# Kernel tuning notes

Measured on AMD Instinct MI355X. Metric: run time of the kernel, lower is better.

## Reference

```python
import jax, jax.numpy as jnp
import numpy as np

B, N, E = 1, 100000, 1250000
IN, OUT = 128, 64


def setup_inputs() -> dict:
    key = jax.random.key(0)
    k = jax.random.split(key, 5)
    x = jax.random.normal(k[0], (B, N, IN), jnp.float32)
    edge_index = jax.random.randint(k[1], (B, 2, E), 0, N, dtype=jnp.int32)
    rank_mapping = jnp.zeros((2, E), jnp.int32)  # single-rank: all zeros
    W1 = jax.random.normal(k[2], (IN, OUT), jnp.float32) / np.sqrt(IN)
    Wp = jax.random.normal(k[3], (2 * OUT, 1), jnp.float32) / np.sqrt(2 * OUT)
    bp = jnp.zeros((1,), jnp.float32)
    bias = jnp.zeros((OUT,), jnp.float32)
    return {"x": x, "edge_index": edge_index, "rank_mapping": rank_mapping,
            "W1": W1, "Wp": Wp, "bp": bp, "bias": bias}


def reference(x, edge_index, rank_mapping, W1, Wp, bp, bias):
    # x: [B, N, IN]; edge_index: [B, 2, E]
    del rank_mapping  # comm routing metadata; identity on a single rank
    n = x.shape[1]
    h = jnp.einsum('bnf,fo->bno', x, W1)          # conv1 (no bias)
    src = edge_index[:, 0, :]                     # [B, E]
    dst = edge_index[:, 1, :]
    h_i = jnp.take_along_axis(h, dst[..., None], axis=1)   # gather at dst
    h_j = jnp.take_along_axis(h, src[..., None], axis=1)   # gather at src
    messages = jnp.concatenate([h_i, h_j], axis=-1)        # [B, E, 2*OUT]
    s = jnp.einsum('bec,co->beo', messages, Wp) + bp       # project_message
    s = jnp.where(s >= 0, s, 0.2 * s)                      # LeakyReLU(0.2)
    numerator = jnp.exp(s)                                 # [B, E, 1]
    seg = jax.vmap(lambda v, i: jax.ops.segment_sum(v, i, num_segments=n))
    denominator = seg(numerator, dst)                      # [B, N, 1]
    # NOTE: original gathers denominator with the *src* indices — replicated.
    denom_e = jnp.take_along_axis(denominator, src[..., None], axis=1)
    alpha = numerator / (denom_e + 1e-16)                  # [B, E, 1]
    out = seg(h_j * alpha, dst)                            # scatter-aggregate
    return out + bias
```

## Files before the change

### kernel.cpp

```cpp
#include <hip/hip_runtime.h>


#define MAXB 1024
#define EPB 4096
#define BIN_CAP 2560

typedef __attribute__((ext_vector_type(8))) short short8v;
typedef __attribute__((ext_vector_type(4))) float floatx4;

static __device__ __forceinline__ float bf2f(unsigned short u) {
    unsigned v = (unsigned)u << 16;
    return __builtin_bit_cast(float, v);
}
static __device__ __forceinline__ unsigned short f2bf(float f) {
    unsigned u = __builtin_bit_cast(unsigned, f);
    u = (u + 0x7FFFu + ((u >> 16) & 1u)) >> 16;
    return (unsigned short)u;
}

__global__ __launch_bounds__(256) void fused_nt_count_kernel(
    const float* __restrict__ x, const float* __restrict__ W1,
    const float* __restrict__ Wp, const int* __restrict__ ei,
    float* __restrict__ h, float* __restrict__ aArr, float* __restrict__ bArr,
    int* __restrict__ C, int N, int E, int G, int B)
{
    __shared__ __align__(16) unsigned short w1b[4][4][4][16][8];
    __shared__ int cnt[MAXB];
    const int tid = threadIdx.x;

    if (blockIdx.x < G) {
        const int g = blockIdx.x;
        for (int i = tid; i < B; i += 256) cnt[i] = 0;
        __syncthreads();
        const int base = g * EPB;
        #pragma unroll
        for (int k = 0; k < EPB / 256; ++k) {
            int e = base + k * 256 + tid;
            if (e < E) atomicAdd(&cnt[ei[E + e] >> 7], 1);
        }
        __syncthreads();
        for (int i = tid; i < B; i += 256) C[(size_t)g * B + i] = cnt[i];
        return;
    }

    for (int i = tid; i < 128 * 64; i += 256) {
        int k = i >> 6, o = i & 63;
        w1b[k >> 5][o >> 4][(k >> 3) & 3][o & 15][k & 7] = f2bf(W1[i]);
    }

    const int w = tid >> 6, lane = tid & 63;
    const int hi = lane >> 4, col = lane & 15;
    float wpa4[4], wpb4[4];
    #pragma unroll
    for (int ot = 0; ot < 4; ++ot) {
        wpa4[ot] = Wp[ot * 16 + col];
        wpb4[ot] = Wp[64 + ot * 16 + col];
    }
    __syncthreads();

    const int n0 = (blockIdx.x - G) * 64 + w * 16;
    int arow = n0 + col; if (arow >= N) arow = N - 1;
    const float* xrow = x + (size_t)arow * 128 + hi * 8;

    floatx4 acc[4] = {{0.f,0.f,0.f,0.f},{0.f,0.f,0.f,0.f},
                      {0.f,0.f,0.f,0.f},{0.f,0.f,0.f,0.f}};
    #pragma unroll
    for (int kb = 0; kb < 4; ++kb) {
        float4 x0 = *reinterpret_cast<const float4*>(xrow + kb * 32);
        float4 x1 = *reinterpret_cast<const float4*>(xrow + kb * 32 + 4);
        short8v af;
        af[0] = (short)f2bf(x0.x); af[1] = (short)f2bf(x0.y);
        af[2] = (short)f2bf(x0.z); af[3] = (short)f2bf(x0.w);
        af[4] = (short)f2bf(x1.x); af[5] = (short)f2bf(x1.y);
        af[6] = (short)f2bf(x1.z); af[7] = (short)f2bf(x1.w);
        #pragma unroll
        for (int ot = 0; ot < 4; ++ot) {
            short8v bf = *reinterpret_cast<const short8v*>(&w1b[kb][ot][hi][col][0]);
            acc[ot] = __builtin_amdgcn_mfma_f32_16x16x32_bf16(af, bf, acc[ot], 0, 0, 0);
        }
    }

    #pragma unroll
    for (int ot = 0; ot < 4; ++ot) {
        #pragma unroll
        for (int r = 0; r < 4; ++r) {
            int n = n0 + hi * 4 + r;
            if (n < N) h[(size_t)n * 64 + ot * 16 + col] = acc[ot][r];
        }
    }
    #pragma unroll
    for (int r = 0; r < 4; ++r) {
        float pa = acc[0][r] * wpa4[0] + acc[1][r] * wpa4[1]
                 + acc[2][r] * wpa4[2] + acc[3][r] * wpa4[3];
        float pb = acc[0][r] * wpb4[0] + acc[1][r] * wpb4[1]
                 + acc[2][r] * wpb4[2] + acc[3][r] * wpb4[3];
        #pragma unroll
        for (int m = 1; m <= 8; m <<= 1) {
            pa += __shfl_xor(pa, m);
            pb += __shfl_xor(pb, m);
        }
        int n = n0 + hi * 4 + r;
        if (col == r && n < N) { aArr[n] = pa; bArr[n] = pb; }
    }
}

__global__ __launch_bounds__(256) void colscan_kernel(
    int* __restrict__ C, int* __restrict__ S, int G, int B)
{
    __shared__ int s[256];
    const int b = blockIdx.x, t = threadIdx.x;
    int g0 = 2 * t, g1 = 2 * t + 1;
    int c0 = (g0 < G) ? C[(size_t)g0 * B + b] : 0;
    int c1 = (g1 < G) ? C[(size_t)g1 * B + b] : 0;
    int v = c0 + c1;
    s[t] = v;
    __syncthreads();
    for (int off = 1; off < 256; off <<= 1) {
        int u = (t >= off) ? s[t - off] : 0;
        __syncthreads();
        s[t] += u;
        __syncthreads();
    }
    int ex = s[t] - v;
    if (g0 < G) C[(size_t)g0 * B + b] = ex;
    if (g1 < G) C[(size_t)g1 * B + b] = ex + c0;
    if (t == 255) S[b] = s[255];
}

__global__ __launch_bounds__(256) void binscan_kernel(
    const int* __restrict__ S, int* __restrict__ binStart,
    int* __restrict__ offsets, int B, int N, int E)
{
    __shared__ int ts[256];
    const int t = threadIdx.x;
    const int chunk = (B + 255) >> 8;
    const int base = t * chunk, lim = min(B, base + chunk);
    int s = 0;
    for (int i = base; i < lim; ++i) s += S[i];
    ts[t] = s;
    __syncthreads();
    for (int off = 1; off < 256; off <<= 1) {
        int u = (t >= off) ? ts[t - off] : 0;
        __syncthreads();
        ts[t] += u;
        __syncthreads();
    }
    int run = ts[t] - s;
    for (int i = base; i < lim; ++i) { binStart[i] = run; run += S[i]; }
    if (t == 0) { binStart[B] = E; offsets[N] = E; }
}

__global__ __launch_bounds__(256) void pass2_kernel(
    const int* __restrict__ ei, const float* __restrict__ aArr,
    const float* __restrict__ bArr, const float* __restrict__ bp,
    const int* __restrict__ C, const int* __restrict__ binStart,
    int2* __restrict__ staging, int E, int G, int B)
{
    __shared__ int cur[MAXB];
    const int g = blockIdx.x, t = threadIdx.x;
    for (int i = t; i < B; i += 256)
        cur[i] = binStart[i] + C[(size_t)g * B + i];
    __syncthreads();
    const float bp0 = bp[0];
    const int base = g * EPB;
    #pragma unroll
    for (int k = 0; k < EPB / 256; ++k) {
        int e = base + k * 256 + t;
        if (e >= E) break;
        int src = ei[e];
        int dst = ei[E + e];
        float s = aArr[dst] + bArr[src] + bp0;
        s = (s >= 0.f) ? s : 0.2f * s;
        float num = __expf(s);
        int bin = dst >> 7;
        int pos = atomicAdd(&cur[bin], 1);
        staging[pos] = make_int2(((dst & 127) << 17) | src, __float_as_int(num));
    }
}

__global__ __launch_bounds__(256) void localsort_kernel(
    const int* __restrict__ binStart, int2* __restrict__ staging,
    int* __restrict__ offsets, int N)
{
    __shared__ int2 sEnt[BIN_CAP];
    __shared__ int sCnt[256], sScan[256], sCur[128];
    const int b = blockIdx.x, t = threadIdx.x;
    const int sBeg = binStart[b];
    const int count = min(binStart[b + 1] - sBeg, BIN_CAP);

    sCnt[t] = 0;
    if (t < 128) sCur[t] = 0;
    __syncthreads();
    for (int i = t; i < count; i += 256) {
        int2 e = staging[sBeg + i];
        sEnt[i] = e;
        atomicAdd(&sCnt[e.x >> 17], 1);
    }
    __syncthreads();
    int v = sCnt[t];
    sScan[t] = v;
    __syncthreads();
    for (int off = 1; off < 256; off <<= 1) {
        int u = (t >= off) ? sScan[t - off] : 0;
        __syncthreads();
        sScan[t] += u;
        __syncthreads();
    }
    int ex = sScan[t] - v;
    __syncthreads();
    sScan[t] = ex;
    const int n0 = b << 7;
    const int Cl = min(128, N - n0);
    if (t < Cl) offsets[n0 + t] = sBeg + ex;
    __syncthreads();
    for (int i = t; i < count; i += 256) {
        int2 e = sEnt[i];
        int dl = e.x >> 17;
        int pos = sBeg + sScan[dl] + atomicAdd(&sCur[dl], 1);
        staging[pos] = make_int2(e.x & 0x1FFFF, e.y);
    }
}

__global__ __launch_bounds__(256) void denom_hh_kernel(
    const int* __restrict__ offsets, const int2* __restrict__ sortedPair,
    float* __restrict__ h, int N)
{
    int gw = (blockIdx.x * blockDim.x + threadIdx.x) >> 6;
    int lane = threadIdx.x & 63;
    if (gw >= N) return;
    int beg = offsets[gw], end = offsets[gw + 1];
    float s = 0.f;
    for (int e = beg + lane; e < end; e += 64) s += __int_as_float(sortedPair[e].y);
    #pragma unroll
    for (int off = 32; off; off >>= 1) s += __shfl_down(s, off);
    s = __shfl(s, 0);
    float inv = 1.f / (s + 1e-16f);
    float hv = h[(size_t)gw * 64 + lane];
    asm volatile("" ::: "memory");
    unsigned short* row = reinterpret_cast<unsigned short*>(h) + (size_t)gw * 128;
    row[lane] = f2bf(hv * inv);
}

__global__ __launch_bounds__(256) void aggregate_kernel(
    const int* __restrict__ offsets, const int2* __restrict__ sortedPair,
    const unsigned* __restrict__ hhW, const float* __restrict__ bias,
    float* __restrict__ out, int N)
{
    int gw = (blockIdx.x * blockDim.x + threadIdx.x) >> 6;
    int lane = threadIdx.x & 63;
    if (gw >= N) return;
    int beg = offsets[gw], end = offsets[gw + 1];
    const int half = lane >> 5;
    const int cp = lane & 31;
    float accx = 0.f, accy = 0.f;
    for (int e0 = beg; e0 < end; e0 += 64) {
        int idx = e0 + lane;
        int2 p = (idx < end) ? sortedPair[idx] : make_int2(0, 0);
        int cnt = min(64, end - e0);
        int j = 0;
        for (; j + 8 <= cnt; j += 8) {
            #pragma unroll
            for (int u = 0; u < 4; ++u) {
                int jj = j + 2 * u + half;
                int s = __shfl(p.x, jj);
                float wv = __shfl(__int_as_float(p.y), jj);
                unsigned g = hhW[(size_t)s * 64 + cp];
                accx = fmaf(bf2f((unsigned short)(g & 0xFFFFu)), wv, accx);
                accy = fmaf(bf2f((unsigned short)(g >> 16)), wv, accy);
            }
        }
        for (; j < cnt; j += 2) {
            int jj = j + half;
            bool v = jj < cnt;
            int s = __shfl(p.x, v ? jj : j);
            float wv = v ? __shfl(__int_as_float(p.y), jj) : 0.f;
            unsigned g = hhW[(size_t)s * 64 + cp];
            accx = fmaf(bf2f((unsigned short)(g & 0xFFFFu)), wv, accx);
            accy = fmaf(bf2f((unsigned short)(g >> 16)), wv, accy);
        }
    }
    accx += __shfl_xor(accx, 32);
    accy += __shfl_xor(accy, 32);
    if (lane < 32) {
        float2 b = reinterpret_cast<const float2*>(bias)[cp];
        float2 o; o.x = accx + b.x; o.y = accy + b.y;
        reinterpret_cast<float2*>(out)[(size_t)gw * 32 + cp] = o;
    }
}

extern "C" void kernel_launch(void* const* d_in, const int* in_sizes, int n_in,
                              void* d_out, int out_size, void* d_ws, size_t ws_size,
                              hipStream_t stream) {
    const float* x    = (const float*)d_in[0];
    const int*   ei   = (const int*)d_in[1];
    const float* W1   = (const float*)d_in[3];
    const float* Wp   = (const float*)d_in[4];
    const float* bp   = (const float*)d_in[5];
    const float* bias = (const float*)d_in[6];
    float* out = (float*)d_out;

    const int N = in_sizes[0] / 128;
    const int E = in_sizes[1] / 2;
    const int B = (N + 127) >> 7;
    const int G = (E + EPB - 1) / EPB;
    const int NTB = (N + 63) / 64;

    float* h        = (float*)d_ws;
    float* aArr     = h + (size_t)N * 64;
    float* bArr     = aArr + N;
    int*   C        = (int*)(bArr + N);
    int*   S        = C + (size_t)G * B;
    int*   binStart = S + B;
    int*   offsets  = binStart + (B + 1);
    int*   stRaw    = offsets + (N + 1);
    stRaw = (int*)(((uintptr_t)stRaw + 7) & ~(uintptr_t)7);
    int2*  staging  = (int2*)stRaw;

    fused_nt_count_kernel<<<G + NTB, 256, 0, stream>>>(
        x, W1, Wp, ei, h, aArr, bArr, C, N, E, G, B);

    colscan_kernel<<<B, 256, 0, stream>>>(C, S, G, B);

    binscan_kernel<<<1, 256, 0, stream>>>(S, binStart, offsets, B, N, E);

    pass2_kernel<<<G, 256, 0, stream>>>(ei, aArr, bArr, bp, C, binStart,
                                        staging, E, G, B);

    localsort_kernel<<<B, 256, 0, stream>>>(binStart, staging, offsets, N);

    denom_hh_kernel<<<(N * 64 + 255) / 256, 256, 0, stream>>>(offsets, staging, h, N);

    aggregate_kernel<<<(N * 64 + 255) / 256, 256, 0, stream>>>(
        offsets, staging, reinterpret_cast<const unsigned*>(h), bias, out, N);
}
```

Before: 132.9 us.

## Fuse denominator scaling into localsort and widen aggregate gathers to 8-byte loads

Removes the separate denom_hh kernel. The per-destination sum of exp scores is now accumulated with shared-memory float atomics inside localsort, and h is scaled and converted to bf16 at the end of that kernel. This saves a launch and a re-read of the sorted pairs. The aggregate kernel now has each lane load 4 bf16 values (uint2) with four edges processed in parallel per wave, which cuts gather instructions but adds a two-step cross-lane reduction. Float atomics in shared memory change the summation order, and the scaling loop adds serial work to each localsort block.

```diff
diff --git a/kernel.cpp b/kernel.cpp
--- a/kernel.cpp
+++ b/kernel.cpp
@@ -180,21 +180,24 @@
 
 __global__ __launch_bounds__(256) void localsort_kernel(
     const int* __restrict__ binStart, int2* __restrict__ staging,
-    int* __restrict__ offsets, int N)
+    int* __restrict__ offsets, float* __restrict__ h, int N)
 {
     __shared__ int2 sEnt[BIN_CAP];
     __shared__ int sCnt[256], sScan[256], sCur[128];
+    __shared__ float dsum[128];
     const int b = blockIdx.x, t = threadIdx.x;
     const int sBeg = binStart[b];
     const int count = min(binStart[b + 1] - sBeg, BIN_CAP);
 
     sCnt[t] = 0;
-    if (t < 128) sCur[t] = 0;
+    if (t < 128) { sCur[t] = 0; dsum[t] = 0.f; }
     __syncthreads();
     for (int i = t; i < count; i += 256) {
         int2 e = staging[sBeg + i];
         sEnt[i] = e;
-        atomicAdd(&sCnt[e.x >> 17], 1);
+        int dl = e.x >> 17;
+        atomicAdd(&sCnt[dl], 1);
+        atomicAdd(&dsum[dl], __int_as_float(e.y));
     }
     __syncthreads();
     int v = sCnt[t];
@@ -219,72 +222,67 @@
         int pos = sBeg + sScan[dl] + atomicAdd(&sCur[dl], 1);
         staging[pos] = make_int2(e.x & 0x1FFFF, e.y);
     }
-}
-
-__global__ __launch_bounds__(256) void denom_hh_kernel(
+
+    const int wv_ = t >> 6, ln = t & 63;
+    for (int dl = wv_; dl < Cl; dl += 4) {
+        int n = n0 + dl;
+        float inv = 1.f / (dsum[dl] + 1e-16f);
+        float hv = h[(size_t)n * 64 + ln];
+        asm volatile("" ::: "memory");
+        reinterpret_cast<unsigned short*>(h)[(size_t)n * 128 + ln] = f2bf(hv * inv);
+    }
+}
+
+__global__ __launch_bounds__(256) void aggregate_kernel(
     const int* __restrict__ offsets, const int2* __restrict__ sortedPair,
-    float* __restrict__ h, int N)
+    const uint2* __restrict__ hhQ, const float* __restrict__ bias,
+    float* __restrict__ out, int N)
 {
     int gw = (blockIdx.x * blockDim.x + threadIdx.x) >> 6;
     int lane = threadIdx.x & 63;
     if (gw >= N) return;
     int beg = offsets[gw], end = offsets[gw + 1];
-    float s = 0.f;
-    for (int e = beg + lane; e < end; e += 64) s += __int_as_float(sortedPair[e].y);
-    #pragma unroll
-    for (int off = 32; off; off >>= 1) s += __shfl_down(s, off);
-    s = __shfl(s, 0);
-    float inv = 1.f / (s + 1e-16f);
-    float hv = h[(size_t)gw * 64 + lane];
-    asm volatile("" ::: "memory");
-    unsigned short* row = reinterpret_cast<unsigned short*>(h) + (size_t)gw * 128;
-    row[lane] = f2bf(hv * inv);
-}
-
-__global__ __launch_bounds__(256) void aggregate_kernel(
-    const int* __restrict__ offsets, const int2* __restrict__ sortedPair,
-    const unsigned* __restrict__ hhW, const float* __restrict__ bias,
-    float* __restrict__ out, int N)
-{
-    int gw = (blockIdx.x * blockDim.x + threadIdx.x) >> 6;
-    int lane = threadIdx.x & 63;
-    if (gw >= N) return;
-    int beg = offsets[gw], end = offsets[gw + 1];
-    const int half = lane >> 5;
-    const int cp = lane & 31;
-    float accx = 0.f, accy = 0.f;
+    const int quarter = lane >> 4;
+    const int cg = lane & 15;
+    float a0 = 0.f, a1 = 0.f, a2 = 0.f, a3 = 0.f;
     for (int e0 = beg; e0 < end; e0 += 64) {
         int idx = e0 + lane;
         int2 p = (idx < end) ? sortedPair[idx] : make_int2(0, 0);
         int cnt = min(64, end - e0);
         int j = 0;
-        for (; j + 8 <= cnt; j += 8) {
+        for (; j + 16 <= cnt; j += 16) {
             #pragma unroll
             for (int u = 0; u < 4; ++u) {
-                int jj = j + 2 * u + half;
+                int jj = j + 4 * u + quarter;
                 int s = __shfl(p.x, jj);
                 float wv = __shfl(__int_as_float(p.y), jj);
-                unsigned g = hhW[(size_t)s * 64 + cp];
-                accx = fmaf(bf2f((unsigned short)(g & 0xFFFFu)), wv, accx);
-                accy = fmaf(bf2f((unsigned short)(g >> 16)), wv, accy);
+                uint2 g = hhQ[(size_t)s * 32 + cg];
+                a0 = fmaf(bf2f((unsigned short)(g.x & 0xFFFFu)), wv, a0);
+                a1 = fmaf(bf2f((unsigned short)(g.x >> 16)), wv, a1);
+                a2 = fmaf(bf2f((unsigned short)(g.y & 0xFFFFu)), wv, a2);
+                a3 = fmaf(bf2f((unsigned short)(g.y >> 16)), wv, a3);
             }
         }
-        for (; j < cnt; j += 2) {
-            int jj = j + half;
-            bool v = jj < cnt;
-            int s = __shfl(p.x, v ? jj : j);
-            float wv = v ? __shfl(__int_as_float(p.y), jj) : 0.f;
-            unsigned g = hhW[(size_t)s * 64 + cp];
-            accx = fmaf(bf2f((unsigned short)(g & 0xFFFFu)), wv, accx);
-            accy = fmaf(bf2f((unsigned short)(g >> 16)), wv, accy);
-        }
-    }
-    accx += __shfl_xor(accx, 32);
-    accy += __shfl_xor(accy, 32);
-    if (lane < 32) {
-        float2 b = reinterpret_cast<const float2*>(bias)[cp];
-        float2 o; o.x = accx + b.x; o.y = accy + b.y;
-        reinterpret_cast<float2*>(out)[(size_t)gw * 32 + cp] = o;
+        for (; j < cnt; j += 4) {
+            int jj = j + quarter;
+            int s = __shfl(p.x, jj);
+            float wv = __shfl(__int_as_float(p.y), jj);
+            uint2 g = hhQ[(size_t)s * 32 + cg];
+            a0 = fmaf(bf2f((unsigned short)(g.x & 0xFFFFu)), wv, a0);
+            a1 = fmaf(bf2f((unsigned short)(g.x >> 16)), wv, a1);
+            a2 = fmaf(bf2f((unsigned short)(g.y & 0xFFFFu)), wv, a2);
+            a3 = fmaf(bf2f((unsigned short)(g.y >> 16)), wv, a3);
+        }
+    }
+    a0 += __shfl_xor(a0, 16); a0 += __shfl_xor(a0, 32);
+    a1 += __shfl_xor(a1, 16); a1 += __shfl_xor(a1, 32);
+    a2 += __shfl_xor(a2, 16); a2 += __shfl_xor(a2, 32);
+    a3 += __shfl_xor(a3, 16); a3 += __shfl_xor(a3, 32);
+    if (lane < 16) {
+        float4 bq = reinterpret_cast<const float4*>(bias)[cg];
+        float4 o;
+        o.x = a0 + bq.x; o.y = a1 + bq.y; o.z = a2 + bq.z; o.w = a3 + bq.w;
+        reinterpret_cast<float4*>(out)[(size_t)gw * 16 + cg] = o;
     }
 }
 
@@ -326,10 +324,8 @@
     pass2_kernel<<<G, 256, 0, stream>>>(ei, aArr, bArr, bp, C, binStart,
                                         staging, E, G, B);
 
-    localsort_kernel<<<B, 256, 0, stream>>>(binStart, staging, offsets, N);
-
-    denom_hh_kernel<<<(N * 64 + 255) / 256, 256, 0, stream>>>(offsets, staging, h, N);
+    localsort_kernel<<<B, 256, 0, stream>>>(binStart, staging, offsets, h, N);
 
     aggregate_kernel<<<(N * 64 + 255) / 256, 256, 0, stream>>>(
-        offsets, staging, reinterpret_cast<const unsigned*>(h), bias, out, N);
-}
+        offsets, staging, reinterpret_cast<const uint2*>(h), bias, out, N);
+}
```

Result: faster. 128.3 us (-3.5%).
